# Kernel tuning notes

Measured on AMD Instinct MI355X. Metric: run time of the kernel, lower is better.

Reference implementation:

```python
import jax, jax.numpy as jnp
import numpy as np

NUM_HEADS = 16

def setup_inputs() -> dict:
    key = jax.random.key(0)
    k1, k2, k3, k4 = jax.random.split(key, 4)
    B, S, E = 4, 2048, 1024
    return {
        "q": jax.random.normal(k1, (B, S, E), dtype=jnp.float32),
        "k": jax.random.normal(k2, (B, S, E), dtype=jnp.float32),
        "v": jax.random.normal(k3, (B, S, E), dtype=jnp.float32),
        "w_out": jax.random.normal(k4, (E, E), dtype=jnp.float32) * (E ** -0.5),
        "b_out": jnp.zeros((E,), dtype=jnp.float32),
    }

def reference(q, k, v, w_out, b_out):
    B, S, E = q.shape
    H = NUM_HEADS
    D = E // H
    scale = D ** -0.5
    # split heads: [B, S, E] -> [B, H, S, D]
    def split(x):
        return x.reshape(B, S, H, D).transpose(0, 2, 1, 3)
    qh, kh, vh = split(q), split(k), split(v)
    scores = jnp.einsum('bhqd,bhkd->bhqk', qh, kh) * scale  # [B,H,S,S]
    weights = jax.nn.softmax(scores, axis=-1)
    # dropout is identity in eval mode
    out = jnp.einsum('bhqk,bhkd->bhqd', weights, vh)
    out = out.transpose(0, 2, 1, 3).reshape(B, S, E)  # merge heads
    return out @ w_out.T + b_out
```

## Files before the change

kernel.cpp:

```cpp
#include <hip/hip_runtime.h>
#include <cstdint>
#include <cstddef>

typedef __attribute__((ext_vector_type(8))) short bf16x8;
typedef __attribute__((ext_vector_type(4))) float f32x4;
typedef __attribute__((ext_vector_type(16))) float f32x16;

#define MFMA16(a, b, c) __builtin_amdgcn_mfma_f32_16x16x32_bf16((a), (b), (c), 0, 0, 0)
#define MFMA32(a, b, c) __builtin_amdgcn_mfma_f32_32x32x16_bf16((a), (b), (c), 0, 0, 0)

constexpr int Bz = 4, S = 2048, E = 1024, H = 16, Dh = 64;
constexpr size_t BSE = (size_t)Bz * S * E;

__device__ __forceinline__ unsigned short f2bf(float f) {
    uint32_t u = __builtin_bit_cast(uint32_t, f);
    u += 0x7FFFu + ((u >> 16) & 1u);
    return (unsigned short)(u >> 16);
}

__device__ __forceinline__ float exp2_fast(float x) {
#if __has_builtin(__builtin_amdgcn_exp2f)
    return __builtin_amdgcn_exp2f(x);
#else
    return exp2f(x);
#endif
}

__device__ __forceinline__ uint32_t pack_bf16(float a, float b) {
    uint32_t ua = __builtin_bit_cast(uint32_t, a) + 0x8000u;
    uint32_t ub = __builtin_bit_cast(uint32_t, b) + 0x8000u;
#if __has_builtin(__builtin_amdgcn_perm)
    return __builtin_amdgcn_perm(ub, ua, 0x07060302u);
#else
    return (ua >> 16) | (ub & 0xFFFF0000u);
#endif
}

__device__ __forceinline__ void gload16(const unsigned short* g, unsigned short* l) {
    __builtin_amdgcn_global_load_lds((const __attribute__((address_space(1))) void*)g,
                                     (__attribute__((address_space(3))) void*)l, 16, 0, 0);
}

__global__ __launch_bounds__(256) void convert_kernel(const float* __restrict__ in,
                                                      unsigned short* __restrict__ out,
                                                      int n4) {
    int i = blockIdx.x * blockDim.x + threadIdx.x;
    if (i < n4) {
        float4 f = ((const float4*)in)[i];
        uint2 u;
        u.x = pack_bf16(f.x, f.y);
        u.y = pack_bf16(f.z, f.w);
        ((uint2*)out)[i] = u;
    }
}

__global__ __launch_bounds__(256) void prep_kv(const float* __restrict__ k,
                                               const float* __restrict__ v,
                                               unsigned short* __restrict__ kb,
                                               unsigned short* __restrict__ vt) {
    __shared__ unsigned short tile[64][65];
    const int b = blockIdx.z, h = blockIdx.y, s0 = blockIdx.x * 64;
    const int r = threadIdx.x >> 2, cb = (threadIdx.x & 3) * 16;
    const size_t off = (size_t)(b * S + s0 + r) * E + h * Dh + cb;

    {
        const float* src = k + off;
        uint32_t o[8];
#pragma unroll
        for (int j = 0; j < 8; ++j) {
            float2 f = *(const float2*)(src + 2 * j);
            o[j] = pack_bf16(f.x, f.y);
        }
        unsigned short* dst = kb + off;
        *(uint4*)(dst) = *(const uint4*)(o);
        *(uint4*)(dst + 8) = *(const uint4*)(o + 4);
    }
    {
        const float* src = v + off;
#pragma unroll
        for (int j = 0; j < 16; j += 4) {
            float4 f = *(const float4*)(src + j);
            tile[cb + j + 0][r] = f2bf(f.x);
            tile[cb + j + 1][r] = f2bf(f.y);
            tile[cb + j + 2][r] = f2bf(f.z);
            tile[cb + j + 3][r] = f2bf(f.w);
        }
    }
    __syncthreads();
    const int dv = threadIdx.x >> 2, seg = (threadIdx.x & 3) * 16;
    unsigned short* dst = vt + (((size_t)(b * H + h) * Dh + dv) * S + s0 + seg);
    *(uint4*)(dst) = *(const uint4*)(&tile[dv][seg]);
    *(uint4*)(dst + 8) = *(const uint4*)(&tile[dv][seg] + 8);
}

constexpr int GSTR = 528;
__global__ __launch_bounds__(256, 2) void attn_kernel(const float* __restrict__ q,
                                                      const unsigned short* __restrict__ kb,
                                                      const unsigned short* __restrict__ vt,
                                                      unsigned short* __restrict__ attn) {
    __shared__ unsigned short smem[18432];

    const int wid = blockIdx.x + 8 * (blockIdx.y + 16 * blockIdx.z);
    const int c_ = wid & 7, j_ = wid >> 3;
    const int bh = c_ * 8 + (j_ >> 3), qblk = j_ & 7;
    const int b = bh >> 4, h = bh & 15;

    const int tid = threadIdx.x;
    const int wave = tid >> 6, lane = tid & 63;
    const int l32 = lane & 31, half = lane >> 5;
    const int x7 = l32 & 7, y4 = l32 >> 3;

    const int q0 = qblk * 256 + wave * 64;
    const float scl = 0.125f * 1.44269504088896f;

    bf16x8 qreg[2][4];
#pragma unroll
    for (int qh = 0; qh < 2; ++qh) {
        const float* qsrc = q + ((size_t)(b * S + q0 + qh * 32 + l32)) * E + h * Dh + half * 8;
#pragma unroll
        for (int t = 0; t < 4; ++t) {
            float4 f0 = *(const float4*)(qsrc + 16 * t);
            float4 f1 = *(const float4*)(qsrc + 16 * t + 4);
            bf16x8 r;
            r[0] = (short)f2bf(f0.x * scl); r[1] = (short)f2bf(f0.y * scl);
            r[2] = (short)f2bf(f0.z * scl); r[3] = (short)f2bf(f0.w * scl);
            r[4] = (short)f2bf(f1.x * scl); r[5] = (short)f2bf(f1.y * scl);
            r[6] = (short)f2bf(f1.z * scl); r[7] = (short)f2bf(f1.w * scl);
            qreg[qh][t] = r;
        }
    }

    f32x16 fzero;
#pragma unroll
    for (int r = 0; r < 16; ++r) fzero[r] = 0.f;
    f32x16 oacc[2][2];
#pragma unroll
    for (int qh = 0; qh < 2; ++qh)
#pragma unroll
        for (int mt = 0; mt < 2; ++mt) oacc[qh][mt] = fzero;
    float lsum[2] = {0.f, 0.f};

    const int row8 = lane >> 3;
    const int sg = (lane & 7) ^ row8;
    const unsigned short* kbase = kb + ((size_t)(b * S)) * E + h * Dh;
    const unsigned short* vtb = vt + ((size_t)(b * H + h) * Dh) * S;

    auto stage = [&](int kt, int bsel) {
        unsigned short* ksb = smem + bsel * 8448;
        unsigned short* vsb = ksb + 4224;
#pragma unroll
        for (int u = 0; u < 2; ++u) {
            const int gi = wave * 2 + u;
            gload16(kbase + (size_t)(kt * 64 + gi * 8 + row8) * E + sg * 8, ksb + gi * GSTR);
            gload16(vtb + (size_t)(gi * 8 + row8) * S + kt * 64 + sg * 8, vsb + gi * GSTR);
        }
    };

    int roff[2];
#pragma unroll
    for (int mt = 0; mt < 2; ++mt) roff[mt] = (mt * 4 + y4) * GSTR + x7 * 64;

    constexpr int NT = S / 64;
    stage(0, 0);

    for (int kt = 0; kt < NT; ++kt) {
        const int cur = kt & 1;
        __syncthreads();
        if (kt + 1 < NT) stage(kt + 1, cur ^ 1);
        const unsigned short* ksb = smem + cur * 8448;
        const unsigned short* vsb = ksb + 4224;

        bf16x8 kfrag[2][4];
#pragma unroll
        for (int mt = 0; mt < 2; ++mt)
#pragma unroll
            for (int t = 0; t < 4; ++t)
                kfrag[mt][t] = *(const bf16x8*)(ksb + roff[mt] + (((t * 2 + half) ^ x7) * 8));

        f32x16 st[2][2];
#pragma unroll
        for (int qh = 0; qh < 2; ++qh)
#pragma unroll
            for (int mt = 0; mt < 2; ++mt) {
                st[qh][mt] = MFMA32(kfrag[mt][0], qreg[qh][0], fzero);
#pragma unroll
                for (int t = 1; t < 4; ++t)
                    st[qh][mt] = MFMA32(kfrag[mt][t], qreg[qh][t], st[qh][mt]);
            }

        uint32_t pkd[2][2][4][2];
#pragma unroll
        for (int qh = 0; qh < 2; ++qh) {
            float ls = 0.f;
#pragma unroll
            for (int mt = 0; mt < 2; ++mt)
#pragma unroll
                for (int g = 0; g < 4; ++g) {
                    float p0 = exp2_fast(st[qh][mt][4 * g + 0]);
                    float p1 = exp2_fast(st[qh][mt][4 * g + 1]);
                    float p2 = exp2_fast(st[qh][mt][4 * g + 2]);
                    float p3 = exp2_fast(st[qh][mt][4 * g + 3]);
                    ls += (p0 + p1) + (p2 + p3);
                    pkd[qh][mt][g][0] = pack_bf16(p0, p1);
                    pkd[qh][mt][g][1] = pack_bf16(p2, p3);
                }
            lsum[qh] += ls;
        }

        bf16x8 vfrag[2][4];
#pragma unroll
        for (int mt = 0; mt < 2; ++mt)
#pragma unroll
            for (int c = 0; c < 4; ++c)
                vfrag[mt][c] = *(const bf16x8*)(vsb + roff[mt] + (((c * 2 + half) ^ x7) * 8));

#pragma unroll
        for (int qh = 0; qh < 2; ++qh)
#pragma unroll
            for (int c = 0; c < 4; ++c) {
                const int ms = c >> 1;
                const int g0 = 2 * (c & 1);
                uint32_t a0 = pkd[qh][ms][g0][0], a1 = pkd[qh][ms][g0][1];
                uint32_t b0 = pkd[qh][ms][g0 + 1][0], b1 = pkd[qh][ms][g0 + 1][1];
                uint32_t snd0 = half ? a0 : b0;
                uint32_t snd1 = half ? a1 : b1;
                uint32_t r0 = (uint32_t)__shfl_xor((int)snd0, 32);
                uint32_t r1 = (uint32_t)__shfl_xor((int)snd1, 32);
                int4 bi;
                bi.x = (int)(half ? r0 : a0);
                bi.y = (int)(half ? r1 : a1);
                bi.z = (int)(half ? b0 : r0);
                bi.w = (int)(half ? b1 : r1);
                bf16x8 bfrag = __builtin_bit_cast(bf16x8, bi);
#pragma unroll
                for (int mt = 0; mt < 2; ++mt)
                    oacc[qh][mt] = MFMA32(vfrag[mt][c], bfrag, oacc[qh][mt]);
            }
    }

    __syncthreads();
    float inv[2];
#pragma unroll
    for (int qh = 0; qh < 2; ++qh) {
        float l = lsum[qh] + (float)__shfl_xor(lsum[qh], 32);
        inv[qh] = 1.0f / l;
    }

    unsigned short* ob = smem + wave * (64 * 72);
#pragma unroll
    for (int qh = 0; qh < 2; ++qh)
#pragma unroll
        for (int mt = 0; mt < 2; ++mt)
#pragma unroll
            for (int g = 0; g < 4; ++g) {
                int dv0 = 8 * g + 4 * half + 32 * mt;
                uint2 w2;
                w2.x = pack_bf16(oacc[qh][mt][4 * g + 0] * inv[qh],
                                 oacc[qh][mt][4 * g + 1] * inv[qh]);
                w2.y = pack_bf16(oacc[qh][mt][4 * g + 2] * inv[qh],
                                 oacc[qh][mt][4 * g + 3] * inv[qh]);
                *(uint2*)(ob + (qh * 32 + l32) * 72 + dv0) = w2;
            }
    __syncthreads();
#pragma unroll
    for (int it = 0; it < 2; ++it) {
        int row = it * 32 + (lane >> 1);
        int seg = (lane & 1) * 32;
        unsigned short* gdst = attn + ((size_t)(b * S + q0 + row)) * E + h * Dh + seg;
#pragma unroll
        for (int j = 0; j < 4; ++j) {
            bf16x8 v8 = *(const bf16x8*)(ob + row * 72 + seg + j * 8);
            *(bf16x8*)(gdst + j * 8) = v8;
        }
    }
}

constexpr int PLD = 40;
__global__ __launch_bounds__(256) void proj_kernel(const unsigned short* __restrict__ A,
                                                   const unsigned short* __restrict__ W,
                                                   const float* __restrict__ bias,
                                                   float* __restrict__ C) {
    __shared__ unsigned short As[128 * PLD];
    __shared__ unsigned short Bs[128 * PLD];
    const int tid = threadIdx.x;
    const int wave = tid >> 6, lane = tid & 63, quad = lane >> 4, l16 = lane & 15;
    const int wm = wave >> 1, wn = wave & 1;
    const int m0 = blockIdx.x * 128, n0 = blockIdx.y * 128;

    f32x4 acc[4][4];
    f32x4 zero = {0.f, 0.f, 0.f, 0.f};
#pragma unroll
    for (int mi = 0; mi < 4; ++mi)
#pragma unroll
        for (int ni = 0; ni < 4; ++ni) acc[mi][ni] = zero;

    const int srow = tid >> 1, scb = (tid & 1) * 16;

    for (int k0 = 0; k0 < 1024; k0 += 32) {
        __syncthreads();
        {
            const uint4* asrc = (const uint4*)(A + (size_t)(m0 + srow) * 1024 + k0 + scb);
            uint4* adst = (uint4*)(As + srow * PLD + scb);
            adst[0] = asrc[0];
            adst[1] = asrc[1];
            const uint4* bsrc = (const uint4*)(W + (size_t)(n0 + srow) * 1024 + k0 + scb);
            uint4* bdst = (uint4*)(Bs + srow * PLD + scb);
            bdst[0] = bsrc[0];
            bdst[1] = bsrc[1];
        }
        __syncthreads();

        bf16x8 af[4], bfr[4];
#pragma unroll
        for (int mi = 0; mi < 4; ++mi)
            af[mi] = *(const bf16x8*)(As + (wm * 64 + mi * 16 + l16) * PLD + quad * 8);
#pragma unroll
        for (int ni = 0; ni < 4; ++ni)
            bfr[ni] = *(const bf16x8*)(Bs + (wn * 64 + ni * 16 + l16) * PLD + quad * 8);
#pragma unroll
        for (int mi = 0; mi < 4; ++mi)
#pragma unroll
            for (int ni = 0; ni < 4; ++ni)
                acc[mi][ni] = MFMA16(af[mi], bfr[ni], acc[mi][ni]);
    }

    float bb[4];
#pragma unroll
    for (int ni = 0; ni < 4; ++ni) bb[ni] = bias[n0 + wn * 64 + ni * 16 + l16];
#pragma unroll
    for (int mi = 0; mi < 4; ++mi) {
        const int row = m0 + wm * 64 + mi * 16 + quad * 4;
#pragma unroll
        for (int ni = 0; ni < 4; ++ni) {
            const int col = n0 + wn * 64 + ni * 16 + l16;
#pragma unroll
            for (int r = 0; r < 4; ++r)
                C[(size_t)(row + r) * 1024 + col] = acc[mi][ni][r] + bb[ni];
        }
    }
}

extern "C" void kernel_launch(void* const* d_in, const int* in_sizes, int n_in,
                              void* d_out, int out_size, void* d_ws, size_t ws_size,
                              hipStream_t stream) {
    const float* q = (const float*)d_in[0];
    const float* k = (const float*)d_in[1];
    const float* v = (const float*)d_in[2];
    const float* w = (const float*)d_in[3];
    const float* bias = (const float*)d_in[4];
    float* out = (float*)d_out;

    unsigned short* ws = (unsigned short*)d_ws;
    unsigned short* kb = ws;
    unsigned short* vt = kb + BSE;
    unsigned short* attnb = vt + BSE;
    unsigned short* wb = attnb + BSE;

    prep_kv<<<dim3(S / 64, H, Bz), dim3(256), 0, stream>>>(k, v, kb, vt);
    {
        int nw4 = (int)((size_t)E * E / 4);
        convert_kernel<<<dim3((nw4 + 255) / 256), dim3(256), 0, stream>>>(w, wb, nw4);
    }
    attn_kernel<<<dim3(S / 256, H, Bz), dim3(256), 0, stream>>>(q, kb, vt, attnb);
    proj_kernel<<<dim3((Bz * S) / 128, E / 128), dim3(256), 0, stream>>>(attnb, wb, bias, out);
}
```

Before: 261.1 us.

## Halve per-wave query rows in attention to raise occupancy, add MFMA priority hints

Each wave in the attention kernel now handles 32 query rows instead of 64, so a block covers 128 queries and the grid doubles. Launch bounds rise from 2 to 4 blocks per SIMD and the shared buffer shrinks, so fewer registers are used per wave and more waves can be resident to hide latency. s_setprio hints are placed around the MFMA sections. In exchange, each K/V tile staged in LDS is reused by half as many queries, which doubles K/V load traffic per query and halves MFMA work per barrier.

```diff
diff --git a/kernel.cpp b/kernel.cpp
--- a/kernel.cpp
+++ b/kernel.cpp
@@ -94,15 +94,15 @@
 }
 
 constexpr int GSTR = 528;
-__global__ __launch_bounds__(256, 2) void attn_kernel(const float* __restrict__ q,
+__global__ __launch_bounds__(256, 4) void attn_kernel(const float* __restrict__ q,
                                                       const unsigned short* __restrict__ kb,
                                                       const unsigned short* __restrict__ vt,
                                                       unsigned short* __restrict__ attn) {
-    __shared__ unsigned short smem[18432];
-
-    const int wid = blockIdx.x + 8 * (blockIdx.y + 16 * blockIdx.z);
+    __shared__ unsigned short smem[16896];
+
+    const int wid = blockIdx.x + 16 * (blockIdx.y + 16 * blockIdx.z);
     const int c_ = wid & 7, j_ = wid >> 3;
-    const int bh = c_ * 8 + (j_ >> 3), qblk = j_ & 7;
+    const int bh = c_ * 8 + (j_ >> 4), qblk = j_ & 15;
     const int b = bh >> 4, h = bh & 15;
 
     const int tid = threadIdx.x;
@@ -110,13 +110,12 @@
     const int l32 = lane & 31, half = lane >> 5;
     const int x7 = l32 & 7, y4 = l32 >> 3;
 
-    const int q0 = qblk * 256 + wave * 64;
+    const int q0 = qblk * 128 + wave * 32;
     const float scl = 0.125f * 1.44269504088896f;
 
-    bf16x8 qreg[2][4];
-#pragma unroll
-    for (int qh = 0; qh < 2; ++qh) {
-        const float* qsrc = q + ((size_t)(b * S + q0 + qh * 32 + l32)) * E + h * Dh + half * 8;
+    bf16x8 qreg[4];
+    {
+        const float* qsrc = q + ((size_t)(b * S + q0 + l32)) * E + h * Dh + half * 8;
 #pragma unroll
         for (int t = 0; t < 4; ++t) {
             float4 f0 = *(const float4*)(qsrc + 16 * t);
@@ -126,19 +125,17 @@
             r[2] = (short)f2bf(f0.z * scl); r[3] = (short)f2bf(f0.w * scl);
             r[4] = (short)f2bf(f1.x * scl); r[5] = (short)f2bf(f1.y * scl);
             r[6] = (short)f2bf(f1.z * scl); r[7] = (short)f2bf(f1.w * scl);
-            qreg[qh][t] = r;
+            qreg[t] = r;
         }
     }
 
     f32x16 fzero;
 #pragma unroll
     for (int r = 0; r < 16; ++r) fzero[r] = 0.f;
-    f32x16 oacc[2][2];
-#pragma unroll
-    for (int qh = 0; qh < 2; ++qh)
-#pragma unroll
-        for (int mt = 0; mt < 2; ++mt) oacc[qh][mt] = fzero;
-    float lsum[2] = {0.f, 0.f};
+    f32x16 oacc[2];
+    oacc[0] = fzero;
+    oacc[1] = fzero;
+    float lsum = 0.f;
 
     const int row8 = lane >> 3;
     const int sg = (lane & 7) ^ row8;
@@ -177,34 +174,33 @@
             for (int t = 0; t < 4; ++t)
                 kfrag[mt][t] = *(const bf16x8*)(ksb + roff[mt] + (((t * 2 + half) ^ x7) * 8));
 
-        f32x16 st[2][2];
-#pragma unroll
-        for (int qh = 0; qh < 2; ++qh)
-#pragma unroll
-            for (int mt = 0; mt < 2; ++mt) {
-                st[qh][mt] = MFMA32(kfrag[mt][0], qreg[qh][0], fzero);
-#pragma unroll
-                for (int t = 1; t < 4; ++t)
-                    st[qh][mt] = MFMA32(kfrag[mt][t], qreg[qh][t], st[qh][mt]);
-            }
-
-        uint32_t pkd[2][2][4][2];
-#pragma unroll
-        for (int qh = 0; qh < 2; ++qh) {
+        f32x16 st[2];
+        __builtin_amdgcn_s_setprio(1);
+#pragma unroll
+        for (int mt = 0; mt < 2; ++mt) {
+            st[mt] = MFMA32(kfrag[mt][0], qreg[0], fzero);
+#pragma unroll
+            for (int t = 1; t < 4; ++t)
+                st[mt] = MFMA32(kfrag[mt][t], qreg[t], st[mt]);
+        }
+        __builtin_amdgcn_s_setprio(0);
+
+        uint32_t pkd[2][4][2];
+        {
             float ls = 0.f;
 #pragma unroll
             for (int mt = 0; mt < 2; ++mt)
 #pragma unroll
                 for (int g = 0; g < 4; ++g) {
-                    float p0 = exp2_fast(st[qh][mt][4 * g + 0]);
-                    float p1 = exp2_fast(st[qh][mt][4 * g + 1]);
-                    float p2 = exp2_fast(st[qh][mt][4 * g + 2]);
-                    float p3 = exp2_fast(st[qh][mt][4 * g + 3]);
+                    float p0 = exp2_fast(st[mt][4 * g + 0]);
+                    float p1 = exp2_fast(st[mt][4 * g + 1]);
+                    float p2 = exp2_fast(st[mt][4 * g + 2]);
+                    float p3 = exp2_fast(st[mt][4 * g + 3]);
                     ls += (p0 + p1) + (p2 + p3);
-                    pkd[qh][mt][g][0] = pack_bf16(p0, p1);
-                    pkd[qh][mt][g][1] = pack_bf16(p2, p3);
+                    pkd[mt][g][0] = pack_bf16(p0, p1);
+                    pkd[mt][g][1] = pack_bf16(p2, p3);
                 }
-            lsum[qh] += ls;
+            lsum += ls;
         }
 
         bf16x8 vfrag[2][4];
@@ -215,57 +211,48 @@
                 vfrag[mt][c] = *(const bf16x8*)(vsb + roff[mt] + (((c * 2 + half) ^ x7) * 8));
 
 #pragma unroll
-        for (int qh = 0; qh < 2; ++qh)
-#pragma unroll
-            for (int c = 0; c < 4; ++c) {
-                const int ms = c >> 1;
-                const int g0 = 2 * (c & 1);
-                uint32_t a0 = pkd[qh][ms][g0][0], a1 = pkd[qh][ms][g0][1];
-                uint32_t b0 = pkd[qh][ms][g0 + 1][0], b1 = pkd[qh][ms][g0 + 1][1];
-                uint32_t snd0 = half ? a0 : b0;
-                uint32_t snd1 = half ? a1 : b1;
-                uint32_t r0 = (uint32_t)__shfl_xor((int)snd0, 32);
-                uint32_t r1 = (uint32_t)__shfl_xor((int)snd1, 32);
-                int4 bi;
-                bi.x = (int)(half ? r0 : a0);
-                bi.y = (int)(half ? r1 : a1);
-                bi.z = (int)(half ? b0 : r0);
-                bi.w = (int)(half ? b1 : r1);
-                bf16x8 bfrag = __builtin_bit_cast(bf16x8, bi);
-#pragma unroll
-                for (int mt = 0; mt < 2; ++mt)
-                    oacc[qh][mt] = MFMA32(vfrag[mt][c], bfrag, oacc[qh][mt]);
-            }
+        for (int c = 0; c < 4; ++c) {
+            const int ms = c >> 1;
+            const int g0 = 2 * (c & 1);
+            uint32_t a0 = pkd[ms][g0][0], a1 = pkd[ms][g0][1];
+            uint32_t b0 = pkd[ms][g0 + 1][0], b1 = pkd[ms][g0 + 1][1];
+            uint32_t snd0 = half ? a0 : b0;
+            uint32_t snd1 = half ? a1 : b1;
+            uint32_t r0 = (uint32_t)__shfl_xor((int)snd0, 32);
+            uint32_t r1 = (uint32_t)__shfl_xor((int)snd1, 32);
+            int4 bi;
+            bi.x = (int)(half ? r0 : a0);
+            bi.y = (int)(half ? r1 : a1);
+            bi.z = (int)(half ? b0 : r0);
+            bi.w = (int)(half ? b1 : r1);
+            bf16x8 bfrag = __builtin_bit_cast(bf16x8, bi);
+            __builtin_amdgcn_s_setprio(1);
+#pragma unroll
+            for (int mt = 0; mt < 2; ++mt)
+                oacc[mt] = MFMA32(vfrag[mt][c], bfrag, oacc[mt]);
+            __builtin_amdgcn_s_setprio(0);
+        }
     }
 
     __syncthreads();
-    float inv[2];
-#pragma unroll
-    for (int qh = 0; qh < 2; ++qh) {
-        float l = lsum[qh] + (float)__shfl_xor(lsum[qh], 32);
-        inv[qh] = 1.0f / l;
-    }
-
-    unsigned short* ob = smem + wave * (64 * 72);
-#pragma unroll
-    for (int qh = 0; qh < 2; ++qh)
-#pragma unroll
-        for (int mt = 0; mt < 2; ++mt)
-#pragma unroll
-            for (int g = 0; g < 4; ++g) {
-                int dv0 = 8 * g + 4 * half + 32 * mt;
-                uint2 w2;
-                w2.x = pack_bf16(oacc[qh][mt][4 * g + 0] * inv[qh],
-                                 oacc[qh][mt][4 * g + 1] * inv[qh]);
-                w2.y = pack_bf16(oacc[qh][mt][4 * g + 2] * inv[qh],
-                                 oacc[qh][mt][4 * g + 3] * inv[qh]);
-                *(uint2*)(ob + (qh * 32 + l32) * 72 + dv0) = w2;
-            }
+    float l = lsum + (float)__shfl_xor(lsum, 32);
+    float inv = 1.0f / l;
+
+    unsigned short* ob = smem + wave * (32 * 72);
+#pragma unroll
+    for (int mt = 0; mt < 2; ++mt)
+#pragma unroll
+        for (int g = 0; g < 4; ++g) {
+            int dv0 = 8 * g + 4 * half + 32 * mt;
+            uint2 w2;
+            w2.x = pack_bf16(oacc[mt][4 * g + 0] * inv, oacc[mt][4 * g + 1] * inv);
+            w2.y = pack_bf16(oacc[mt][4 * g + 2] * inv, oacc[mt][4 * g + 3] * inv);
+            *(uint2*)(ob + l32 * 72 + dv0) = w2;
+        }
     __syncthreads();
-#pragma unroll
-    for (int it = 0; it < 2; ++it) {
-        int row = it * 32 + (lane >> 1);
-        int seg = (lane & 1) * 32;
+    {
+        const int row = lane >> 1;
+        const int seg = (lane & 1) * 32;
         unsigned short* gdst = attn + ((size_t)(b * S + q0 + row)) * E + h * Dh + seg;
 #pragma unroll
         for (int j = 0; j < 4; ++j) {
@@ -361,6 +348,6 @@
         int nw4 = (int)((size_t)E * E / 4);
         convert_kernel<<<dim3((nw4 + 255) / 256), dim3(256), 0, stream>>>(w, wb, nw4);
     }
-    attn_kernel<<<dim3(S / 256, H, Bz), dim3(256), 0, stream>>>(q, kb, vt, attnb);
+    attn_kernel<<<dim3(S / 128, H, Bz), dim3(256), 0, stream>>>(q, kb, vt, attnb);
     proj_kernel<<<dim3((Bz * S) / 128, E / 128), dim3(256), 0, stream>>>(attnb, wb, bias, out);
 }
```

After: 268.8 us. 3.0% more time.

## Software-pipeline PV MFMAs one tile behind and raise wave priority around MFMAs

Applied to the files above, without the earlier changes.

Each iteration's P·V matrix multiplies now run one iteration late: the V fragments and packed, shuffled probability operands are kept in registers (vfragP/bfragP). They are consumed after the next tile's QK^T MFMAs, with a final drain after the loop. This lets the exp/pack/shuffle softmax work of one tile interleave with matrix-core work of the neighbouring tile. MFMA blocks are also wrapped in s_setprio(1) so waves issuing matrix work get scheduling priority. The carried fragments add about 64 live VGPRs per lane, which may lower occupancy or cause spills.

```diff
diff --git a/kernel.cpp b/kernel.cpp
--- a/kernel.cpp
+++ b/kernel.cpp
@@ -160,6 +160,9 @@
 #pragma unroll
     for (int mt = 0; mt < 2; ++mt) roff[mt] = (mt * 4 + y4) * GSTR + x7 * 64;
 
+    bf16x8 vfragP[2][4];
+    int4 bfragP[2][4];
+
     constexpr int NT = S / 64;
     stage(0, 0);
 
@@ -178,6 +181,7 @@
                 kfrag[mt][t] = *(const bf16x8*)(ksb + roff[mt] + (((t * 2 + half) ^ x7) * 8));
 
         f32x16 st[2][2];
+        __builtin_amdgcn_s_setprio(1);
 #pragma unroll
         for (int qh = 0; qh < 2; ++qh)
 #pragma unroll
@@ -187,6 +191,27 @@
                 for (int t = 1; t < 4; ++t)
                     st[qh][mt] = MFMA32(kfrag[mt][t], qreg[qh][t], st[qh][mt]);
             }
+        __builtin_amdgcn_s_setprio(0);
+
+        if (kt > 0) {
+            __builtin_amdgcn_s_setprio(1);
+#pragma unroll
+            for (int qh = 0; qh < 2; ++qh)
+#pragma unroll
+                for (int c = 0; c < 4; ++c) {
+                    bf16x8 bfrag = __builtin_bit_cast(bf16x8, bfragP[qh][c]);
+#pragma unroll
+                    for (int mt = 0; mt < 2; ++mt)
+                        oacc[qh][mt] = MFMA32(vfragP[mt][c], bfrag, oacc[qh][mt]);
+                }
+            __builtin_amdgcn_s_setprio(0);
+        }
+
+#pragma unroll
+        for (int mt = 0; mt < 2; ++mt)
+#pragma unroll
+            for (int c = 0; c < 4; ++c)
+                vfragP[mt][c] = *(const bf16x8*)(vsb + roff[mt] + (((c * 2 + half) ^ x7) * 8));
 
         uint32_t pkd[2][2][4][2];
 #pragma unroll
@@ -206,13 +231,6 @@
                 }
             lsum[qh] += ls;
         }
-
-        bf16x8 vfrag[2][4];
-#pragma unroll
-        for (int mt = 0; mt < 2; ++mt)
-#pragma unroll
-            for (int c = 0; c < 4; ++c)
-                vfrag[mt][c] = *(const bf16x8*)(vsb + roff[mt] + (((c * 2 + half) ^ x7) * 8));
 
 #pragma unroll
         for (int qh = 0; qh < 2; ++qh)
@@ -231,12 +249,21 @@
                 bi.y = (int)(half ? r1 : a1);
                 bi.z = (int)(half ? b0 : r0);
                 bi.w = (int)(half ? b1 : r1);
-                bf16x8 bfrag = __builtin_bit_cast(bf16x8, bi);
-#pragma unroll
-                for (int mt = 0; mt < 2; ++mt)
-                    oacc[qh][mt] = MFMA32(vfrag[mt][c], bfrag, oacc[qh][mt]);
+                bfragP[qh][c] = bi;
             }
     }
+
+    __builtin_amdgcn_s_setprio(1);
+#pragma unroll
+    for (int qh = 0; qh < 2; ++qh)
+#pragma unroll
+        for (int c = 0; c < 4; ++c) {
+            bf16x8 bfrag = __builtin_bit_cast(bf16x8, bfragP[qh][c]);
+#pragma unroll
+            for (int mt = 0; mt < 2; ++mt)
+                oacc[qh][mt] = MFMA32(vfragP[mt][c], bfrag, oacc[qh][mt]);
+        }
+    __builtin_amdgcn_s_setprio(0);
 
     __syncthreads();
     float inv[2];
```

Result: slower. 279.5 us (+7.0%).

## Double-buffer projection GEMM tiles with direct global-to-LDS loads

Applied to the files above, without the earlier changes.

The output-projection GEMM now keeps two shared-memory buffers. While the current K-tile is consumed by MFMAs, the next tile is prefetched with the gload16 direct-to-LDS helper, which replaces the register round-trip copy and drops one barrier per iteration. The cost is an unpadded 32-element LDS row stride, which may cause bank conflicts on fragment reads. Correctness also relies on the barrier draining the outstanding async loads.

```diff
diff --git a/kernel.cpp b/kernel.cpp
--- a/kernel.cpp
+++ b/kernel.cpp
@@ -275,13 +275,11 @@
     }
 }
 
-constexpr int PLD = 40;
 __global__ __launch_bounds__(256) void proj_kernel(const unsigned short* __restrict__ A,
                                                    const unsigned short* __restrict__ W,
                                                    const float* __restrict__ bias,
                                                    float* __restrict__ C) {
-    __shared__ unsigned short As[128 * PLD];
-    __shared__ unsigned short Bs[128 * PLD];
+    __shared__ unsigned short smem[16384];
     const int tid = threadIdx.x;
     const int wave = tid >> 6, lane = tid & 63, quad = lane >> 4, l16 = lane & 15;
     const int wm = wave >> 1, wn = wave & 1;
@@ -294,29 +292,39 @@
 #pragma unroll
         for (int ni = 0; ni < 4; ++ni) acc[mi][ni] = zero;
 
-    const int srow = tid >> 1, scb = (tid & 1) * 16;
-
-    for (int k0 = 0; k0 < 1024; k0 += 32) {
+    const int row16 = lane >> 2, slot = lane & 3;
+    const unsigned short* Abase = A + (size_t)m0 * 1024;
+    const unsigned short* Wbase = W + (size_t)n0 * 1024;
+
+    auto stage = [&](int k0, int bsel) {
+        unsigned short* as = smem + bsel * 8192;
+        unsigned short* bs = as + 4096;
+#pragma unroll
+        for (int i = 0; i < 2; ++i) {
+            const int g = wave * 2 + i;
+            const int r = g * 16 + row16;
+            gload16(Abase + (size_t)r * 1024 + k0 + slot * 8, as + g * 512);
+            gload16(Wbase + (size_t)r * 1024 + k0 + slot * 8, bs + g * 512);
+        }
+    };
+
+    constexpr int NT = 1024 / 32;
+    stage(0, 0);
+
+    for (int t = 0; t < NT; ++t) {
+        const int cur = t & 1;
         __syncthreads();
-        {
-            const uint4* asrc = (const uint4*)(A + (size_t)(m0 + srow) * 1024 + k0 + scb);
-            uint4* adst = (uint4*)(As + srow * PLD + scb);
-            adst[0] = asrc[0];
-            adst[1] = asrc[1];
-            const uint4* bsrc = (const uint4*)(W + (size_t)(n0 + srow) * 1024 + k0 + scb);
-            uint4* bdst = (uint4*)(Bs + srow * PLD + scb);
-            bdst[0] = bsrc[0];
-            bdst[1] = bsrc[1];
-        }
-        __syncthreads();
+        if (t + 1 < NT) stage((t + 1) * 32, cur ^ 1);
+        const unsigned short* as = smem + cur * 8192;
+        const unsigned short* bs = as + 4096;
 
         bf16x8 af[4], bfr[4];
 #pragma unroll
         for (int mi = 0; mi < 4; ++mi)
-            af[mi] = *(const bf16x8*)(As + (wm * 64 + mi * 16 + l16) * PLD + quad * 8);
+            af[mi] = *(const bf16x8*)(as + (wm * 64 + mi * 16 + l16) * 32 + quad * 8);
 #pragma unroll
         for (int ni = 0; ni < 4; ++ni)
-            bfr[ni] = *(const bf16x8*)(Bs + (wn * 64 + ni * 16 + l16) * PLD + quad * 8);
+            bfr[ni] = *(const bf16x8*)(bs + (wn * 64 + ni * 16 + l16) * 32 + quad * 8);
 #pragma unroll
         for (int mi = 0; mi < 4; ++mi)
 #pragma unroll
```

Measured after the change: 252.7 us (median of 2 runs). -3.2%, faster.
